# Optimization experiments

Measured on AMD Instinct MI355X. Metric: run time of the kernel, lower is better.

The kernel has to match this reference:

```python
import jax, jax.numpy as jnp
import numpy as np
import math

EMB = 512
HEADS = 8
FM = 56
WS = 7


def _relative_position_index(ws):
    coords = np.stack(np.meshgrid(np.arange(ws), np.arange(ws), indexing='ij')).reshape(2, -1)
    rel = coords[:, :, None] - coords[:, None, :]            # [2, ws^2, ws^2]
    rel = rel.transpose(1, 2, 0)                              # [ws^2, ws^2, 2]
    rel = rel + np.abs(rel.min())                             # shift to >= 0 (adds ws-1)
    rel[:, :, 0] = rel[:, :, 0] * (2 * ws - 1)
    return rel.sum(-1)                                        # [ws^2, ws^2] int

REL_IDX = jnp.asarray(_relative_position_index(WS))


def setup_inputs() -> dict:
    key = jax.random.key(0)
    ks = jax.random.split(key, 8)
    B, L, E = 16, FM * FM, EMB
    scale = 0.02
    return {
        'x': jax.random.normal(ks[0], (B, L, E), dtype=jnp.float32),
        'q_w': jax.random.normal(ks[1], (E, E), dtype=jnp.float32) * scale,
        'q_b': jax.random.normal(ks[2], (E,), dtype=jnp.float32) * scale,
        'k_w': jax.random.normal(ks[3], (E, E), dtype=jnp.float32) * scale,
        'k_b': jax.random.normal(ks[4], (E,), dtype=jnp.float32) * scale,
        'v_w': jax.random.normal(ks[5], (E, E), dtype=jnp.float32) * scale,
        'v_b': jax.random.normal(ks[6], (E,), dtype=jnp.float32) * scale,
        'bias_table': jax.random.normal(ks[7], ((2 * WS - 1) ** 2, HEADS), dtype=jnp.float32) * scale,
    }


def reference(x, q_w, q_b, k_w, k_b, v_w, v_b, bias_table):
    B, L, E = x.shape
    nh, d, ws = HEADS, E // HEADS, WS
    n = ws * ws
    # Faithful to the torch code: reshape (NOT channels-last transpose), then window partition
    xr = x.reshape(B, E, FM, FM)
    w = xr.reshape(B, FM // ws, ws, FM // ws, ws, E)
    w = jnp.transpose(w, (0, 1, 3, 2, 4, 5)).reshape(B, -1, ws, ws, E)  # [B, nW, ws, ws, E]
    nW = w.shape[1]
    # Linear projections (torch Linear: x @ W.T + b)
    q = (w @ q_w.T + q_b).reshape(B, nW, nh, n, d)
    k = (w @ k_w.T + k_b).reshape(B, nW, nh, n, d)
    v = (w @ v_w.T + v_b).reshape(B, nW, nh, n, d)
    # Relative position bias: [nh, n, n]
    bias = bias_table[REL_IDX.reshape(-1)].reshape(n, n, nh).transpose(2, 0, 1)
    scores = jnp.einsum('bwhqd,bwhkd->bwhqk', q, k) / math.sqrt(d)
    scores = scores + bias[None, None]
    attn = jax.nn.softmax(scores, axis=-1)
    out = jnp.einsum('bwhqk,bwhkd->bwhqd', attn, v)
    return out.reshape(B, L, E)
```

## Files before the change

kernel.cpp:

```cpp
#include <hip/hip_runtime.h>

typedef __attribute__((ext_vector_type(8))) short short8;
typedef __attribute__((ext_vector_type(4))) short short4v;
typedef __attribute__((ext_vector_type(4))) float float4v;
typedef __attribute__((ext_vector_type(8))) __bf16 bf16x8;

#define LDS_PQ 57344
#define LDS_PK 107520
#define LDS_BIAS 157696
#define LDS_TOTAL 163104

__device__ __forceinline__ unsigned short f2bf(float f) {
  unsigned u = __float_as_uint(f);
  u += 0x7FFFu + ((u >> 16) & 1u);
  return (unsigned short)(u >> 16);
}

__device__ __forceinline__ int pswz(int s) { return ((s ^ (s >> 3)) & 7) << 4; }

__global__ void wconv_kernel(const float* __restrict__ qw, const float* __restrict__ kw,
                             const float* __restrict__ vw, short* __restrict__ out) {
  int idx = blockIdx.x * 256 + threadIdx.x;
  int g = idx >> 15;
  int rem = idx & 32767;
  int lane = rem & 63;
  int n01 = (rem >> 6) & 1;
  int w   = (rem >> 7) & 15;
  int kk  = rem >> 11;
  int o  = w * 32 + n01 * 16 + (lane & 15);
  int k0 = kk * 32 + (lane >> 4) * 8;
  const float* src = (g == 0) ? qw : (g == 1) ? kw : vw;
  const float* p = src + o * 512 + k0;
  float4v v0 = *(const float4v*)(p);
  float4v v1 = *(const float4v*)(p + 4);
  short8 o8;
  o8[0] = (short)f2bf(v0.x); o8[1] = (short)f2bf(v0.y);
  o8[2] = (short)f2bf(v0.z); o8[3] = (short)f2bf(v0.w);
  o8[4] = (short)f2bf(v1.x); o8[5] = (short)f2bf(v1.y);
  o8[6] = (short)f2bf(v1.z); o8[7] = (short)f2bf(v1.w);
  *(short8*)(out + idx * 8) = o8;
}

__global__ __launch_bounds__(1024, 4) void wattn_kernel(
    const float* __restrict__ x, const short* __restrict__ wcvt,
    const float* __restrict__ qb, const float* __restrict__ kb, const float* __restrict__ vb,
    const float* __restrict__ btab, float* __restrict__ out) {
  __shared__ __align__(16) char sm[LDS_TOTAL];
  const int tid  = threadIdx.x;
  const int lane = tid & 63;
  const int wave = tid >> 6;
  const int bwi  = blockIdx.x;
  const int bb   = bwi >> 6, wi = bwi & 63;
  const int l15  = lane & 15;
  const int l4   = lane >> 4;
  const int ig   = l4 * 4;

  for (int i = tid; i < 169 * 8; i += 1024)
    *(float*)(sm + LDS_BIAS + i * 4) = btab[i];

  {
    const float* xb = x + (size_t)bb * (3136 * 512);
    const int whi = (wi >> 3) * 7, wlo = (wi & 7) * 7;
    for (int idx = tid; idx < 49 * 128; idx += 1024) {
      int t = idx >> 7, c4 = idx & 127;
      int yt = (t * 37) >> 8, xt = t - yt * 7;
      int l = (whi + yt) * 56 + wlo + xt;
      float4v v = *(const float4v*)(xb + l * 512 + c4 * 4);
      short4v o;
      o.x = (short)f2bf(v.x); o.y = (short)f2bf(v.y);
      o.z = (short)f2bf(v.z); o.w = (short)f2bf(v.w);
      int byte = t * 1024 + c4 * 8;
      *(short4v*)(sm + (byte ^ ((t & 7) << 4))) = o;
    }
  }
  __syncthreads();

  const int wcol = wave * 32;
  const int ck   = l4 * 16;

  int xbase[4], xsw[4];
#pragma unroll
  for (int mt = 0; mt < 4; ++mt) {
    int row = mt * 16 + l15;
    xbase[mt] = row * 1024;
    xsw[mt]   = (row & 7) << 4;
  }

  const short* wgb0 = wcvt + wave * 1024 + lane * 8;

#define LDW(OFF) __builtin_bit_cast(bf16x8, *(const short8*)(wgb + (OFF)))
#define GEMM_PHASE(KIDX, W0, W1)                                                          \
  do {                                                                                    \
    const int c_ = (KIDX) * 64 + ck;                                                      \
    bf16x8 x0_ = __builtin_bit_cast(bf16x8, *(const short8*)(sm + xbase[0] + (c_ ^ xsw[0]))); \
    bf16x8 x1_ = __builtin_bit_cast(bf16x8, *(const short8*)(sm + xbase[1] + (c_ ^ xsw[1]))); \
    bf16x8 x2_ = __builtin_bit_cast(bf16x8, *(const short8*)(sm + xbase[2] + (c_ ^ xsw[2]))); \
    bf16x8 x3_ = __builtin_bit_cast(bf16x8, *(const short8*)(sm + xbase[3] + (c_ ^ xsw[3]))); \
    acc[0][0] = __builtin_amdgcn_mfma_f32_16x16x32_bf16(W0, x0_, acc[0][0], 0, 0, 0);     \
    acc[1][0] = __builtin_amdgcn_mfma_f32_16x16x32_bf16(W1, x0_, acc[1][0], 0, 0, 0);     \
    acc[0][1] = __builtin_amdgcn_mfma_f32_16x16x32_bf16(W0, x1_, acc[0][1], 0, 0, 0);     \
    acc[1][1] = __builtin_amdgcn_mfma_f32_16x16x32_bf16(W1, x1_, acc[1][1], 0, 0, 0);     \
    acc[0][2] = __builtin_amdgcn_mfma_f32_16x16x32_bf16(W0, x2_, acc[0][2], 0, 0, 0);     \
    acc[1][2] = __builtin_amdgcn_mfma_f32_16x16x32_bf16(W1, x2_, acc[1][2], 0, 0, 0);     \
    acc[0][3] = __builtin_amdgcn_mfma_f32_16x16x32_bf16(W0, x3_, acc[0][3], 0, 0, 0);     \
    acc[1][3] = __builtin_amdgcn_mfma_f32_16x16x32_bf16(W1, x3_, acc[1][3], 0, 0, 0);     \
  } while (0)

  for (int g = 0; g < 3; ++g) {
    const short* wgb = wgb0 + g * 262144;
    const float* bias = (g == 0) ? qb : (g == 1) ? kb : vb;
    float4v acc[2][4];
#pragma unroll
    for (int nt = 0; nt < 2; ++nt)
#pragma unroll
      for (int mt = 0; mt < 4; ++mt) acc[nt][mt] = (float4v)0.f;

    bf16x8 wa0 = LDW(0),         wa1 = LDW(512);
    bf16x8 wb0 = LDW(16384),     wb1 = LDW(16384 + 512);
    bf16x8 wc0, wc1, wd0, wd1;

#pragma unroll 1
    for (int kk = 0; kk < 16; kk += 4) {
      wc0 = LDW(((kk + 2) & 15) * 16384); wc1 = LDW(((kk + 2) & 15) * 16384 + 512);
      GEMM_PHASE(kk, wa0, wa1);
      wd0 = LDW(((kk + 3) & 15) * 16384); wd1 = LDW(((kk + 3) & 15) * 16384 + 512);
      GEMM_PHASE(kk + 1, wb0, wb1);
      wa0 = LDW(((kk + 4) & 15) * 16384); wa1 = LDW(((kk + 4) & 15) * 16384 + 512);
      GEMM_PHASE(kk + 2, wc0, wc1);
      wb0 = LDW(((kk + 5) & 15) * 16384); wb1 = LDW(((kk + 5) & 15) * 16384 + 512);
      GEMM_PHASE(kk + 3, wd0, wd1);
    }

    if (g < 2) {
      const int base = (g == 0) ? LDS_PQ : LDS_PK;
      const float qs = (g == 0) ? 0.125f : 1.0f;
#pragma unroll
      for (int nt = 0; nt < 2; ++nt) {
        int o0 = wcol + nt * 16 + ig;
        float4v bv = *(const float4v*)(bias + o0);
        int dd0 = o0 & 63, sg = o0 >> 6;
#pragma unroll
        for (int mt = 0; mt < 4; ++mt) {
          int t = mt * 16 + l15;
          if (t < 49) {
            int s = t * 8 + sg;
            short4v pk;
#pragma unroll
            for (int r = 0; r < 4; ++r) pk[r] = (short)f2bf((acc[nt][mt][r] + bv[r]) * qs);
            *(short4v*)(sm + base + ((s * 128 + dd0 * 2) ^ pswz(s))) = pk;
          }
        }
      }
    } else {
      __syncthreads();
#pragma unroll
      for (int nt = 0; nt < 2; ++nt) {
        int o0 = wcol + nt * 16 + ig;
        float4v bv = *(const float4v*)(bias + o0);
        int dd0 = o0 & 63, sg = o0 >> 6;
#pragma unroll
        for (int mt = 0; mt < 4; ++mt) {
          int t = mt * 16 + l15;
          if (t < 49) {
            int s = t * 8 + sg;
            int h2 = (s * 1339) >> 16;
            int colb = h2 * 112 + (s - h2 * 49) * 2;
#pragma unroll
            for (int r = 0; r < 4; ++r) {
              int dd = dd0 + r;
              *(unsigned short*)(sm + ((dd * 896 + colb) ^ ((dd & 7) << 4))) =
                  f2bf(acc[nt][mt][r] + bv[r]);
            }
          }
        }
      }
      if (tid < 512) {
        int h2 = tid >> 6, dd = tid & 63;
        int rowb = dd * 896 + h2 * 112;
        int swz = (dd & 7) << 4;
#pragma unroll
        for (int q = 49; q < 56; ++q)
          *(unsigned short*)(sm + ((rowb + q * 2) ^ swz)) = 0;
      }
    }
  }

  const int h  = wave & 7;
  const int mh = wave >> 3;
  const float* bias_f = (const float*)(sm + LDS_BIAS);

  float4v sc[4][2];
#pragma unroll
  for (int jt = 0; jt < 4; ++jt)
#pragma unroll
    for (int it = 0; it < 2; ++it) sc[jt][it] = (float4v)0.f;

#pragma unroll
  for (int ks = 0; ks < 2; ++ks) {
    const int dd = ks * 32 + l4 * 8;
    bf16x8 kf[4], qf[2];
#pragma unroll
    for (int jt = 0; jt < 4; ++jt) {
      int s = h * 49 + jt * 16 + l15;
      int flat = s * 128 + dd * 2;
      kf[jt] = __builtin_bit_cast(bf16x8, *(const short8*)(sm + LDS_PK + (flat ^ pswz(s))));
    }
#pragma unroll
    for (int it = 0; it < 2; ++it) {
      int s = h * 49 + (mh * 2 + it) * 16 + l15;
      int flat = s * 128 + dd * 2;
      qf[it] = __builtin_bit_cast(bf16x8, *(const short8*)(sm + LDS_PQ + (flat ^ pswz(s))));
    }
#pragma unroll
    for (int jt = 0; jt < 4; ++jt)
#pragma unroll
      for (int it = 0; it < 2; ++it)
        sc[jt][it] = __builtin_amdgcn_mfma_f32_16x16x32_bf16(kf[jt], qf[it], sc[jt][it], 0, 0, 0);
  }

#pragma unroll
  for (int it = 0; it < 2; ++it) {
    int i = (mh * 2 + it) * 16 + l15;
    int yi = (i * 37) >> 8, xi = i - yi * 7;
    float mx = -1e30f;
#pragma unroll
    for (int jt = 0; jt < 4; ++jt)
#pragma unroll
      for (int r = 0; r < 4; ++r) {
        int j = jt * 16 + ig + r;
        float v = -1e30f;
        if (i < 49 && j < 49) {
          int yj = (j * 37) >> 8, xj = j - yj * 7;
          int idx = (yi - yj + 6) * 13 + (xi - xj + 6);
          v = sc[jt][it][r] + bias_f[idx * 8 + h];
        }
        sc[jt][it][r] = v;
        mx = fmaxf(mx, v);
      }
    mx = fmaxf(mx, __shfl_xor(mx, 16));
    mx = fmaxf(mx, __shfl_xor(mx, 32));
    float ssum = 0.f;
#pragma unroll
    for (int jt = 0; jt < 4; ++jt)
#pragma unroll
      for (int r = 0; r < 4; ++r) {
        float e = __expf(sc[jt][it][r] - mx);
        sc[jt][it][r] = e;
        ssum += e;
      }
    ssum += __shfl_xor(ssum, 16);
    ssum += __shfl_xor(ssum, 32);
    float inv = 1.f / ssum;
#pragma unroll
    for (int jt = 0; jt < 4; ++jt)
#pragma unroll
      for (int r = 0; r < 4; ++r) sc[jt][it][r] *= inv;
  }

#pragma unroll
  for (int it = 0; it < 2; ++it) {
    int i = (mh * 2 + it) * 16 + l15;
    if (i < 49) {
      int s = h * 49 + i;
      int rowb = s * 128;
      int swz = pswz(s);
#pragma unroll
      for (int jt = 0; jt < 4; ++jt) {
        short4v pk;
#pragma unroll
        for (int r = 0; r < 4; ++r) pk[r] = (short)f2bf(sc[jt][it][r]);
        *(short4v*)(sm + LDS_PQ + ((rowb + jt * 32 + ig * 2) ^ swz)) = pk;
      }
    }
  }

  __syncthreads();

  float4v oacc[4][2];
#pragma unroll
  for (int dt = 0; dt < 4; ++dt)
#pragma unroll
    for (int tt = 0; tt < 2; ++tt) oacc[dt][tt] = (float4v)0.f;

#pragma unroll
  for (int ks = 0; ks < 2; ++ks) {
    const int tp0 = ks * 32 + l4 * 8;
    bf16x8 vf[4], af[2];
#pragma unroll
    for (int dt = 0; dt < 4; ++dt) {
      int dd = dt * 16 + l15;
      vf[dt] = __builtin_bit_cast(bf16x8,
          *(const short8*)(sm + ((dd * 896 + h * 112 + tp0 * 2) ^ ((dd & 7) << 4))));
    }
#pragma unroll
    for (int tt = 0; tt < 2; ++tt) {
      int t = (mh * 2 + tt) * 16 + l15;
      int tr = (t > 48) ? 48 : t;
      int s = h * 49 + tr;
      af[tt] = __builtin_bit_cast(bf16x8,
          *(const short8*)(sm + LDS_PQ + ((s * 128 + tp0 * 2) ^ pswz(s))));
    }
#pragma unroll
    for (int dt = 0; dt < 4; ++dt)
#pragma unroll
      for (int tt = 0; tt < 2; ++tt)
        oacc[dt][tt] = __builtin_amdgcn_mfma_f32_16x16x32_bf16(vf[dt], af[tt], oacc[dt][tt], 0, 0, 0);
  }

  float* op = out + (size_t)bwi * 25088 + h * 3136;
#pragma unroll
  for (int tt = 0; tt < 2; ++tt) {
    int t = (mh * 2 + tt) * 16 + l15;
    if (t < 49) {
#pragma unroll
      for (int dt = 0; dt < 4; ++dt)
        *(float4v*)(op + t * 64 + dt * 16 + ig) = oacc[dt][tt];
    }
  }
#undef LDW
#undef GEMM_PHASE
}

extern "C" void kernel_launch(void* const* d_in, const int* in_sizes, int n_in,
                              void* d_out, int out_size, void* d_ws, size_t ws_size,
                              hipStream_t stream) {
  const float* x    = (const float*)d_in[0];
  const float* q_w  = (const float*)d_in[1];
  const float* q_b  = (const float*)d_in[2];
  const float* k_w  = (const float*)d_in[3];
  const float* k_b  = (const float*)d_in[4];
  const float* v_w  = (const float*)d_in[5];
  const float* v_b  = (const float*)d_in[6];
  const float* btab = (const float*)d_in[7];
  short* wcvt = (short*)d_ws;

  hipLaunchKernelGGL(wconv_kernel, dim3(384), dim3(256), 0, stream, q_w, k_w, v_w, wcvt);
  hipLaunchKernelGGL(wattn_kernel, dim3(1024), dim3(1024), 0, stream,
                     x, wcvt, q_b, k_b, v_b, btab, (float*)d_out);
}
```

Measured before the change: 165.1 us.

## Retile QKV projection per wave to 64 output columns by 32 rows

Each wave now computes a 64-column (one head) by 32-row tile of the QKV projection instead of a 32-column by 64-row tile. The weight fragment layout in the conversion kernel is reordered to match, and the pipelined weight prefetch now loads four fragments per k-step with double buffering. This halves the per-wave LDS reads of x and doubles the per-wave global weight loads. Because two waves now share each weight tile, L2 weight traffic rises, and prefetch depth drops from two stages to one.

New measurement: 191.0 us. +15.7%, slower.

```diff
diff --git a/kernel.cpp b/kernel.cpp
--- a/kernel.cpp
+++ b/kernel.cpp
@@ -24,10 +24,9 @@
   int g = idx >> 15;
   int rem = idx & 32767;
   int lane = rem & 63;
-  int n01 = (rem >> 6) & 1;
-  int w   = (rem >> 7) & 15;
-  int kk  = rem >> 11;
-  int o  = w * 32 + n01 * 16 + (lane & 15);
+  int frag = (rem >> 6) & 31;
+  int kk   = rem >> 11;
+  int o  = (frag >> 2) * 64 + (frag & 3) * 16 + (lane & 15);
   int k0 = kk * 32 + (lane >> 4) * 8;
   const float* src = (g == 0) ? qw : (g == 1) ? kw : vw;
   const float* p = src + o * 512 + k0;
@@ -54,6 +53,8 @@
   const int l15  = lane & 15;
   const int l4   = lane >> 4;
   const int ig   = l4 * 4;
+  const int h    = wave & 7;
+  const int mh   = wave >> 3;
 
   for (int i = tid; i < 169 * 8; i += 1024)
     *(float*)(sm + LDS_BIAS + i * 4) = btab[i];
@@ -75,75 +76,74 @@
   }
   __syncthreads();
 
-  const int wcol = wave * 32;
-  const int ck   = l4 * 16;
-
-  int xbase[4], xsw[4];
-#pragma unroll
-  for (int mt = 0; mt < 4; ++mt) {
-    int row = mt * 16 + l15;
+  const int ck = l4 * 16;
+
+  int xbase[2], xsw[2];
+#pragma unroll
+  for (int mt = 0; mt < 2; ++mt) {
+    int row = mh * 32 + mt * 16 + l15;
     xbase[mt] = row * 1024;
     xsw[mt]   = (row & 7) << 4;
   }
 
-  const short* wgb0 = wcvt + wave * 1024 + lane * 8;
-
-#define LDW(OFF) __builtin_bit_cast(bf16x8, *(const short8*)(wgb + (OFF)))
-#define GEMM_PHASE(KIDX, W0, W1)                                                          \
-  do {                                                                                    \
-    const int c_ = (KIDX) * 64 + ck;                                                      \
-    bf16x8 x0_ = __builtin_bit_cast(bf16x8, *(const short8*)(sm + xbase[0] + (c_ ^ xsw[0]))); \
-    bf16x8 x1_ = __builtin_bit_cast(bf16x8, *(const short8*)(sm + xbase[1] + (c_ ^ xsw[1]))); \
-    bf16x8 x2_ = __builtin_bit_cast(bf16x8, *(const short8*)(sm + xbase[2] + (c_ ^ xsw[2]))); \
-    bf16x8 x3_ = __builtin_bit_cast(bf16x8, *(const short8*)(sm + xbase[3] + (c_ ^ xsw[3]))); \
-    acc[0][0] = __builtin_amdgcn_mfma_f32_16x16x32_bf16(W0, x0_, acc[0][0], 0, 0, 0);     \
-    acc[1][0] = __builtin_amdgcn_mfma_f32_16x16x32_bf16(W1, x0_, acc[1][0], 0, 0, 0);     \
-    acc[0][1] = __builtin_amdgcn_mfma_f32_16x16x32_bf16(W0, x1_, acc[0][1], 0, 0, 0);     \
-    acc[1][1] = __builtin_amdgcn_mfma_f32_16x16x32_bf16(W1, x1_, acc[1][1], 0, 0, 0);     \
-    acc[0][2] = __builtin_amdgcn_mfma_f32_16x16x32_bf16(W0, x2_, acc[0][2], 0, 0, 0);     \
-    acc[1][2] = __builtin_amdgcn_mfma_f32_16x16x32_bf16(W1, x2_, acc[1][2], 0, 0, 0);     \
-    acc[0][3] = __builtin_amdgcn_mfma_f32_16x16x32_bf16(W0, x3_, acc[0][3], 0, 0, 0);     \
-    acc[1][3] = __builtin_amdgcn_mfma_f32_16x16x32_bf16(W1, x3_, acc[1][3], 0, 0, 0);     \
+  const short* wgb0 = wcvt + h * 2048 + lane * 8;
+
+#define LDW4(DST, KIDX)                                                                     \
+  do {                                                                                      \
+    const short* p_ = wgb + ((KIDX) & 15) * 16384;                                          \
+    DST[0] = __builtin_bit_cast(bf16x8, *(const short8*)(p_));                              \
+    DST[1] = __builtin_bit_cast(bf16x8, *(const short8*)(p_ + 512));                        \
+    DST[2] = __builtin_bit_cast(bf16x8, *(const short8*)(p_ + 1024));                       \
+    DST[3] = __builtin_bit_cast(bf16x8, *(const short8*)(p_ + 1536));                       \
+  } while (0)
+
+#define GEMM_PHASE(KIDX, W)                                                                 \
+  do {                                                                                      \
+    const int c_ = (KIDX) * 64 + ck;                                                        \
+    bf16x8 x0_ = __builtin_bit_cast(bf16x8, *(const short8*)(sm + xbase[0] + (c_ ^ xsw[0])));\
+    bf16x8 x1_ = __builtin_bit_cast(bf16x8, *(const short8*)(sm + xbase[1] + (c_ ^ xsw[1])));\
+    acc[0][0] = __builtin_amdgcn_mfma_f32_16x16x32_bf16(W[0], x0_, acc[0][0], 0, 0, 0);     \
+    acc[1][0] = __builtin_amdgcn_mfma_f32_16x16x32_bf16(W[1], x0_, acc[1][0], 0, 0, 0);     \
+    acc[2][0] = __builtin_amdgcn_mfma_f32_16x16x32_bf16(W[2], x0_, acc[2][0], 0, 0, 0);     \
+    acc[3][0] = __builtin_amdgcn_mfma_f32_16x16x32_bf16(W[3], x0_, acc[3][0], 0, 0, 0);     \
+    acc[0][1] = __builtin_amdgcn_mfma_f32_16x16x32_bf16(W[0], x1_, acc[0][1], 0, 0, 0);     \
+    acc[1][1] = __builtin_amdgcn_mfma_f32_16x16x32_bf16(W[1], x1_, acc[1][1], 0, 0, 0);     \
+    acc[2][1] = __builtin_amdgcn_mfma_f32_16x16x32_bf16(W[2], x1_, acc[2][1], 0, 0, 0);     \
+    acc[3][1] = __builtin_amdgcn_mfma_f32_16x16x32_bf16(W[3], x1_, acc[3][1], 0, 0, 0);     \
   } while (0)
 
   for (int g = 0; g < 3; ++g) {
     const short* wgb = wgb0 + g * 262144;
     const float* bias = (g == 0) ? qb : (g == 1) ? kb : vb;
-    float4v acc[2][4];
-#pragma unroll
-    for (int nt = 0; nt < 2; ++nt)
-#pragma unroll
-      for (int mt = 0; mt < 4; ++mt) acc[nt][mt] = (float4v)0.f;
-
-    bf16x8 wa0 = LDW(0),         wa1 = LDW(512);
-    bf16x8 wb0 = LDW(16384),     wb1 = LDW(16384 + 512);
-    bf16x8 wc0, wc1, wd0, wd1;
+    float4v acc[4][2];
+#pragma unroll
+    for (int nt = 0; nt < 4; ++nt)
+#pragma unroll
+      for (int mt = 0; mt < 2; ++mt) acc[nt][mt] = (float4v)0.f;
+
+    bf16x8 wA[4], wB[4];
+    LDW4(wA, 0);
 
 #pragma unroll 1
-    for (int kk = 0; kk < 16; kk += 4) {
-      wc0 = LDW(((kk + 2) & 15) * 16384); wc1 = LDW(((kk + 2) & 15) * 16384 + 512);
-      GEMM_PHASE(kk, wa0, wa1);
-      wd0 = LDW(((kk + 3) & 15) * 16384); wd1 = LDW(((kk + 3) & 15) * 16384 + 512);
-      GEMM_PHASE(kk + 1, wb0, wb1);
-      wa0 = LDW(((kk + 4) & 15) * 16384); wa1 = LDW(((kk + 4) & 15) * 16384 + 512);
-      GEMM_PHASE(kk + 2, wc0, wc1);
-      wb0 = LDW(((kk + 5) & 15) * 16384); wb1 = LDW(((kk + 5) & 15) * 16384 + 512);
-      GEMM_PHASE(kk + 3, wd0, wd1);
+    for (int kk = 0; kk < 16; kk += 2) {
+      LDW4(wB, kk + 1);
+      GEMM_PHASE(kk, wA);
+      LDW4(wA, kk + 2);
+      GEMM_PHASE(kk + 1, wB);
     }
 
     if (g < 2) {
       const int base = (g == 0) ? LDS_PQ : LDS_PK;
       const float qs = (g == 0) ? 0.125f : 1.0f;
 #pragma unroll
-      for (int nt = 0; nt < 2; ++nt) {
-        int o0 = wcol + nt * 16 + ig;
-        float4v bv = *(const float4v*)(bias + o0);
-        int dd0 = o0 & 63, sg = o0 >> 6;
-#pragma unroll
-        for (int mt = 0; mt < 4; ++mt) {
-          int t = mt * 16 + l15;
+      for (int nt = 0; nt < 4; ++nt) {
+        int dd0 = nt * 16 + ig;
+        float4v bv = *(const float4v*)(bias + h * 64 + dd0);
+#pragma unroll
+        for (int mt = 0; mt < 2; ++mt) {
+          int t = mh * 32 + mt * 16 + l15;
           if (t < 49) {
-            int s = t * 8 + sg;
+            int s = t * 8 + h;
             short4v pk;
 #pragma unroll
             for (int r = 0; r < 4; ++r) pk[r] = (short)f2bf((acc[nt][mt][r] + bv[r]) * qs);
@@ -154,15 +154,14 @@
     } else {
       __syncthreads();
 #pragma unroll
-      for (int nt = 0; nt < 2; ++nt) {
-        int o0 = wcol + nt * 16 + ig;
-        float4v bv = *(const float4v*)(bias + o0);
-        int dd0 = o0 & 63, sg = o0 >> 6;
-#pragma unroll
-        for (int mt = 0; mt < 4; ++mt) {
-          int t = mt * 16 + l15;
+      for (int nt = 0; nt < 4; ++nt) {
+        int dd0 = nt * 16 + ig;
+        float4v bv = *(const float4v*)(bias + h * 64 + dd0);
+#pragma unroll
+        for (int mt = 0; mt < 2; ++mt) {
+          int t = mh * 32 + mt * 16 + l15;
           if (t < 49) {
-            int s = t * 8 + sg;
+            int s = t * 8 + h;
             int h2 = (s * 1339) >> 16;
             int colb = h2 * 112 + (s - h2 * 49) * 2;
 #pragma unroll
@@ -185,8 +184,6 @@
     }
   }
 
-  const int h  = wave & 7;
-  const int mh = wave >> 3;
   const float* bias_f = (const float*)(sm + LDS_BIAS);
 
   float4v sc[4][2];
@@ -317,7 +314,7 @@
         *(float4v*)(op + t * 64 + dt * 16 + ig) = oacc[dt][tt];
     }
   }
-#undef LDW
+#undef LDW4
 #undef GEMM_PHASE
 }
 
```
